# Kernel optimization log

Measured on AMD Instinct MI355X. Metric: run time of the kernel, lower is better.

## Reference

```python
import jax, jax.numpy as jnp
import numpy as np
import math

B, S, D, H = 2, 2048, 1024, 16
DK = D // H


def setup_inputs() -> dict:
    key = jax.random.key(0)
    ks = jax.random.split(key, 5)
    scale = 0.02
    x = jax.random.normal(ks[0], (B, S, D), dtype=jnp.float32)
    wq = jax.random.normal(ks[1], (D, D), dtype=jnp.float32) * scale
    wk = jax.random.normal(ks[2], (D, D), dtype=jnp.float32) * scale
    wv = jax.random.normal(ks[3], (D, D), dtype=jnp.float32) * scale
    wo = jax.random.normal(ks[4], (D, D), dtype=jnp.float32) * scale
    bq = jnp.zeros((D,), jnp.float32)
    bk = jnp.zeros((D,), jnp.float32)
    bv = jnp.zeros((D,), jnp.float32)
    bo = jnp.zeros((D,), jnp.float32)
    # causal mask: mask==0 positions are filled with -inf in the original
    mask = jnp.tril(jnp.ones((S, S), dtype=bool))[None, None]  # [1,1,S,S]
    return {"x": x, "mask": mask, "wq": wq, "bq": bq, "wk": wk, "bk": bk,
            "wv": wv, "bv": bv, "wo": wo, "bo": bo}


def reference(x, mask, wq, bq, wk, bk, wv, bv, wo, bo):
    b, sl, d = x.shape
    # torch Linear: y = x @ W^T + b
    def proj(w, bias):
        y = jnp.einsum('bsd,ed->bse', x, w) + bias
        return y.reshape(b, sl, H, DK).transpose(0, 2, 1, 3)  # [B,H,S,DK]
    q = proj(wq, bq)
    k = proj(wk, bk)
    v = proj(wv, bv)
    sc = jnp.einsum('bhqd,bhkd->bhqk', q, k) / math.sqrt(DK)  # [B,H,S,S]
    sc = jnp.where(mask, sc, -jnp.inf)
    aw = jax.nn.softmax(sc, axis=-1)
    # dropout is identity in eval mode (reference baseline)
    ao = jnp.einsum('bhqk,bhkd->bhqd', aw, v)
    ao = ao.transpose(0, 2, 1, 3).reshape(b, sl, d)
    out = jnp.einsum('bsd,ed->bse', ao, wo) + bo
    return out
```

## Files before the change

### kernel.cpp

```cpp
#include <hip/hip_runtime.h>
#include <cstdint>
#include <cstddef>

#define Bb 2
#define Ss 2048
#define Dd 1024
#define Hh 16
#define DKk 64

typedef unsigned short ushort_t;
typedef __bf16 bf16x8 __attribute__((ext_vector_type(8)));
typedef float f32x4 __attribute__((ext_vector_type(4)));
typedef unsigned short us8 __attribute__((ext_vector_type(8)));
typedef unsigned short us4 __attribute__((ext_vector_type(4)));

__device__ __forceinline__ ushort_t f2bf(float f) {
  __bf16 h = (__bf16)f;
  return __builtin_bit_cast(unsigned short, h);
}

__device__ __forceinline__ void gload_lds16(const void* g, void* l) {
  __builtin_amdgcn_global_load_lds(
      (__attribute__((address_space(1))) void*)(g),
      (__attribute__((address_space(3))) void*)(l),
      16, 0, 0);
}

__global__ __launch_bounds__(256) void cast_k(const float* __restrict__ s,
                                              ushort_t* __restrict__ d, int n8) {
  const int i = blockIdx.x * 256 + threadIdx.x;
  if (i >= n8) return;
  const float4* sp = (const float4*)s;
  float4 a = sp[2 * i], b = sp[2 * i + 1];
  us8 o;
  o[0] = f2bf(a.x); o[1] = f2bf(a.y); o[2] = f2bf(a.z); o[3] = f2bf(a.w);
  o[4] = f2bf(b.x); o[5] = f2bf(b.y); o[6] = f2bf(b.z); o[7] = f2bf(b.w);
  ((us8*)d)[i] = o;
}

template <int MODE>
__global__ __launch_bounds__(256) void gemm_k(
    const ushort_t* __restrict__ A, const ushort_t* __restrict__ W,
    const float* __restrict__ b0, const float* __restrict__ b1,
    const float* __restrict__ b2,
    ushort_t* __restrict__ oQ, ushort_t* __restrict__ oK,
    ushort_t* __restrict__ oVT, float* __restrict__ oF) {
  constexpr int Kd = 1024;
  __shared__ ushort_t As[128 * 32];
  __shared__ ushort_t Bs[128 * 32];
  const int tid = threadIdx.x;
  const int lane = tid & 63;
  const int wave = tid >> 6;
  const int m0 = blockIdx.y * 128;
  const int n0 = blockIdx.x * 128;
  const int lr = lane & 15;
  const int lg = lane >> 4;
  const int srow = lane >> 2;
  const int scol = (lane & 3) * 8;
  const int ar = (wave >> 1) * 64;
  const int bc = (wave & 1) * 64;

  f32x4 acc[4][4] = {};

  for (int kt = 0; kt < Kd / 32; ++kt) {
    const int k0 = kt * 32;
#pragma unroll
    for (int c = 0; c < 2; ++c) {
      const int seg = wave * 2 + c;
      const int row = seg * 16 + srow;
      gload_lds16(A + (size_t)(m0 + row) * Kd + k0 + scol, (char*)As + seg * 1024);
      gload_lds16(W + (size_t)(n0 + row) * Kd + k0 + scol, (char*)Bs + seg * 1024);
    }
    __syncthreads();
    bf16x8 af[4], bfr[4];
#pragma unroll
    for (int i = 0; i < 4; ++i)
      af[i] = *(const bf16x8*)&As[(ar + i * 16 + lr) * 32 + lg * 8];
#pragma unroll
    for (int j = 0; j < 4; ++j)
      bfr[j] = *(const bf16x8*)&Bs[(bc + j * 16 + lr) * 32 + lg * 8];
#pragma unroll
    for (int i = 0; i < 4; ++i)
#pragma unroll
      for (int j = 0; j < 4; ++j)
        acc[i][j] = __builtin_amdgcn_mfma_f32_16x16x32_bf16(af[i], bfr[j],
                                                            acc[i][j], 0, 0, 0);
    __syncthreads();
  }

#pragma unroll
  for (int i = 0; i < 4; ++i) {
    const int mrow = m0 + ar + i * 16 + lg * 4;
#pragma unroll
    for (int j = 0; j < 4; ++j) {
      const int n = n0 + bc + j * 16 + lr;
      if (MODE == 0) {
        const int sel = n >> 10;
        const int nn = n & 1023;
        const float bias = (sel == 0 ? b0 : sel == 1 ? b1 : b2)[nn];
        const int h = nn >> 6, dk = nn & 63;
        const int bidx = mrow >> 11;
        const int s = mrow & 2047;
        const int bh = bidx * Hh + h;
        if (sel == 2) {
          us4 pk;
#pragma unroll
          for (int r = 0; r < 4; ++r) pk[r] = f2bf(acc[i][j][r] + bias);
          *(us4*)&oVT[((size_t)bh * DKk + dk) * Ss + s] = pk;
        } else {
          ushort_t* dst = (sel == 0) ? oQ : oK;
          const float mul = (sel == 0) ? 0.1803368842f : 1.0f;
#pragma unroll
          for (int r = 0; r < 4; ++r)
            dst[((size_t)bh * Ss + (s + r)) * DKk + dk] =
                f2bf((acc[i][j][r] + bias) * mul);
        }
      } else {
        const float bias = b0[n];
#pragma unroll
        for (int r = 0; r < 4; ++r)
          oF[(size_t)(mrow + r) * Dd + n] = acc[i][j][r] + bias;
      }
    }
  }
}

__global__ __launch_bounds__(256, 4) void attn_k(const ushort_t* __restrict__ Qg,
                                                 const ushort_t* __restrict__ Kg,
                                                 const ushort_t* __restrict__ Vt,
                                                 ushort_t* __restrict__ AO) {
  __shared__ ushort_t Ks[2][64 * 64];
  __shared__ ushort_t Pl[4][16 * 72];
  const int tid = threadIdx.x, lane = tid & 63, wave = tid >> 6;
  const int bx = blockIdx.x;
  const int bh = bx & 31;
  const int r_ = bx >> 8;
  const int sub = (bx >> 5) & 7;
  const int g = (3 - r_) * 8 + ((r_ & 1) ? 7 - sub : sub);
  const int lr = lane & 15, lg = lane >> 4;
  const ushort_t* Qp = Qg + (size_t)bh * Ss * DKk;
  const ushort_t* Kp = Kg + (size_t)bh * Ss * DKk;
  const ushort_t* Vp = Vt + (size_t)bh * DKk * Ss;
  ushort_t* P = Pl[wave];
  const int s_row = lane >> 3;
  const int s_slot = (lane & 7) ^ s_row;
  const int sw = lr & 7;
  const int q0 = g * 64 + wave * 16;
  const int nt = g + 1;

  auto stageK = [&](int t, int buf) {
    const int rb = wave * 16;
#pragma unroll
    for (int c = 0; c < 2; ++c)
      gload_lds16(Kp + (size_t)(t * 64 + rb + c * 8 + s_row) * DKk + s_slot * 8,
                  &Ks[buf][(rb + c * 8) * 64]);
  };

  stageK(0, 0);

  bf16x8 qf[2];
#pragma unroll
  for (int ks = 0; ks < 2; ++ks)
    qf[ks] = *(const bf16x8*)&Qp[(size_t)(q0 + lr) * DKk + ks * 32 + lg * 8];

  f32x4 o[4] = {};
  float m_ = -3e38f, l_ = 0.f;

  __syncthreads();

  for (int t = 0; t < nt; ++t) {
    const int cb = t & 1;
    if (t + 1 < nt) stageK(t + 1, cb ^ 1);
    const int j0 = t * 64;
    const bool diag = (t == nt - 1);
    const int nct = diag ? wave + 1 : 4;

    bf16x8 vt[4][2];
#pragma unroll
    for (int dj = 0; dj < 4; ++dj)
#pragma unroll
      for (int ksp = 0; ksp < 2; ++ksp)
        vt[dj][ksp] = *(const bf16x8*)&Vp[(size_t)(dj * 16 + lr) * Ss + j0 +
                                          ksp * 32 + lg * 8];

    f32x4 sc[4];
#pragma unroll
    for (int ct = 0; ct < 4; ++ct) {
      if (ct < nct) {
        const int krow = ct * 16 + lr;
        const bf16x8 k0v = *(const bf16x8*)&Ks[cb][krow * 64 + ((lg ^ sw) * 8)];
        const bf16x8 k1v =
            *(const bf16x8*)&Ks[cb][krow * 64 + (((4 | lg) ^ sw) * 8)];
        f32x4 z = {};
        z = __builtin_amdgcn_mfma_f32_16x16x32_bf16(k0v, qf[0], z, 0, 0, 0);
        z = __builtin_amdgcn_mfma_f32_16x16x32_bf16(k1v, qf[1], z, 0, 0, 0);
        sc[ct] = z;
      }
    }
    if (diag) {
#pragma unroll
      for (int ct = 0; ct < 4; ++ct)
        if (ct == nct - 1)
#pragma unroll
          for (int r = 0; r < 4; ++r)
            if (lg * 4 + r > lr) sc[ct][r] = -1e30f;
    }

    float mx = -3e38f;
#pragma unroll
    for (int ct = 0; ct < 4; ++ct)
      if (ct < nct)
#pragma unroll
        for (int r = 0; r < 4; ++r) mx = fmaxf(mx, sc[ct][r]);
    mx = fmaxf(mx, __shfl_xor(mx, 16, 64));
    mx = fmaxf(mx, __shfl_xor(mx, 32, 64));
    const float mnew = fmaxf(m_, mx);
    const float fs = __builtin_exp2f(m_ - mnew);
    m_ = mnew;
    float ls = 0.f;
#pragma unroll
    for (int ct = 0; ct < 4; ++ct) {
      if (ct < nct) {
        float p0 = __builtin_exp2f(sc[ct][0] - mnew);
        float p1 = __builtin_exp2f(sc[ct][1] - mnew);
        float p2 = __builtin_exp2f(sc[ct][2] - mnew);
        float p3 = __builtin_exp2f(sc[ct][3] - mnew);
        ls += (p0 + p1) + (p2 + p3);
        us4 pk;
        pk[0] = f2bf(p0); pk[1] = f2bf(p1); pk[2] = f2bf(p2); pk[3] = f2bf(p3);
        *(us4*)&P[lr * 72 + ct * 16 + lg * 4] = pk;
      } else {
        us4 zz = {};
        *(us4*)&P[lr * 72 + ct * 16 + lg * 4] = zz;
      }
    }
    ls += __shfl_xor(ls, 16, 64);
    ls += __shfl_xor(ls, 32, 64);
    l_ = l_ * fs + ls;

    float fso[4];
#pragma unroll
    for (int r = 0; r < 4; ++r) fso[r] = __shfl(fs, lg * 4 + r, 64);
#pragma unroll
    for (int dj = 0; dj < 4; ++dj)
#pragma unroll
      for (int r = 0; r < 4; ++r) o[dj][r] *= fso[r];

    asm volatile("s_waitcnt lgkmcnt(0)" ::: "memory");
    bf16x8 pa[2];
#pragma unroll
    for (int ksp = 0; ksp < 2; ++ksp)
      pa[ksp] = *(const bf16x8*)&P[lr * 72 + ksp * 32 + lg * 8];
#pragma unroll
    for (int dj = 0; dj < 4; ++dj)
#pragma unroll
      for (int ksp = 0; ksp < 2; ++ksp)
        o[dj] = __builtin_amdgcn_mfma_f32_16x16x32_bf16(pa[ksp], vt[dj][ksp],
                                                        o[dj], 0, 0, 0);

    __syncthreads();
  }

  const int bb = bh >> 4, hh = bh & 15;
#pragma unroll
  for (int r = 0; r < 4; ++r) {
    const float lq = __shfl(l_, lg * 4 + r, 64);
    const float inv = 1.0f / lq;
    const size_t m = (size_t)bb * Ss + q0 + lg * 4 + r;
#pragma unroll
    for (int dj = 0; dj < 4; ++dj)
      AO[m * Dd + hh * 64 + dj * 16 + lr] = f2bf(o[dj][r] * inv);
  }
}

extern "C" void kernel_launch(void* const* d_in, const int* in_sizes, int n_in,
                              void* d_out, int out_size, void* d_ws, size_t ws_size,
                              hipStream_t stream) {
  const float* x  = (const float*)d_in[0];
  const float* wq = (const float*)d_in[2];
  const float* bq = (const float*)d_in[3];
  const float* wk = (const float*)d_in[4];
  const float* bk = (const float*)d_in[5];
  const float* wv = (const float*)d_in[6];
  const float* bv = (const float*)d_in[7];
  const float* wo = (const float*)d_in[8];
  const float* bo = (const float*)d_in[9];

  ushort_t* ws   = (ushort_t*)d_ws;
  ushort_t* xb   = ws;
  ushort_t* wqkv = xb + 4096 * 1024;
  ushort_t* wob  = wqkv + 3072 * 1024;
  ushort_t* Qb   = wob + 1024 * 1024;
  ushort_t* Kb   = Qb + 4194304;
  ushort_t* VTb  = Kb + 4194304;
  ushort_t* AOb  = xb;

  cast_k<<<2048, 256, 0, stream>>>(x, xb, 524288);
  cast_k<<<512, 256, 0, stream>>>(wq, wqkv, 131072);
  cast_k<<<512, 256, 0, stream>>>(wk, wqkv + 1048576, 131072);
  cast_k<<<512, 256, 0, stream>>>(wv, wqkv + 2097152, 131072);
  cast_k<<<512, 256, 0, stream>>>(wo, wob, 131072);

  gemm_k<0><<<dim3(24, 32), 256, 0, stream>>>(xb, wqkv, bq, bk, bv, Qb, Kb, VTb,
                                              nullptr);
  attn_k<<<1024, 256, 0, stream>>>(Qb, Kb, VTb, AOb);
  gemm_k<1><<<dim3(8, 32), 256, 0, stream>>>(AOb, wob, bo, nullptr, nullptr,
                                             nullptr, nullptr, nullptr,
                                             (float*)d_out);
}
```

Before: 151.2 us.

## Compute softmax row sums via MFMA and transpose PV output layout

Replaces the per-lane row-sum accumulation and cross-lane shuffles with an MFMA against a ones vector, which accumulates the softmax denominator directly in the accumulator layout. The PV MFMA operands are swapped so each lane holds a full query row in its accumulator. This removes the shuffles for rescale factors and denominators and allows a vectorized 4-element store of the output. It adds two extra MFMAs per tile and depends on the transposed accumulator layout matching the per-lane running max.

```diff
diff --git a/kernel.cpp b/kernel.cpp
--- a/kernel.cpp
+++ b/kernel.cpp
@@ -163,8 +163,13 @@
   for (int ks = 0; ks < 2; ++ks)
     qf[ks] = *(const bf16x8*)&Qp[(size_t)(q0 + lr) * DKk + ks * 32 + lg * 8];
 
+  bf16x8 onesv;
+#pragma unroll
+  for (int e = 0; e < 8; ++e) onesv[e] = (__bf16)1.0f;
+
   f32x4 o[4] = {};
-  float m_ = -3e38f, l_ = 0.f;
+  f32x4 l4 = {};
+  float m_ = -3e38f;
 
   __syncthreads();
 
@@ -217,15 +222,13 @@
     const float mnew = fmaxf(m_, mx);
     const float fs = __builtin_exp2f(m_ - mnew);
     m_ = mnew;
-    float ls = 0.f;
 #pragma unroll
     for (int ct = 0; ct < 4; ++ct) {
       if (ct < nct) {
-        float p0 = __builtin_exp2f(sc[ct][0] - mnew);
-        float p1 = __builtin_exp2f(sc[ct][1] - mnew);
-        float p2 = __builtin_exp2f(sc[ct][2] - mnew);
-        float p3 = __builtin_exp2f(sc[ct][3] - mnew);
-        ls += (p0 + p1) + (p2 + p3);
+        float p0 = __builtin_exp2f(sc[ct][0] - m_);
+        float p1 = __builtin_exp2f(sc[ct][1] - m_);
+        float p2 = __builtin_exp2f(sc[ct][2] - m_);
+        float p3 = __builtin_exp2f(sc[ct][3] - m_);
         us4 pk;
         pk[0] = f2bf(p0); pk[1] = f2bf(p1); pk[2] = f2bf(p2); pk[3] = f2bf(p3);
         *(us4*)&P[lr * 72 + ct * 16 + lg * 4] = pk;
@@ -234,42 +237,41 @@
         *(us4*)&P[lr * 72 + ct * 16 + lg * 4] = zz;
       }
     }
-    ls += __shfl_xor(ls, 16, 64);
-    ls += __shfl_xor(ls, 32, 64);
-    l_ = l_ * fs + ls;
-
-    float fso[4];
-#pragma unroll
-    for (int r = 0; r < 4; ++r) fso[r] = __shfl(fs, lg * 4 + r, 64);
+
 #pragma unroll
     for (int dj = 0; dj < 4; ++dj)
 #pragma unroll
-      for (int r = 0; r < 4; ++r) o[dj][r] *= fso[r];
+      for (int r = 0; r < 4; ++r) o[dj][r] *= fs;
+    l4[0] *= fs;
 
     asm volatile("s_waitcnt lgkmcnt(0)" ::: "memory");
     bf16x8 pa[2];
 #pragma unroll
     for (int ksp = 0; ksp < 2; ++ksp)
       pa[ksp] = *(const bf16x8*)&P[lr * 72 + ksp * 32 + lg * 8];
+
+#pragma unroll
+    for (int ksp = 0; ksp < 2; ++ksp)
+      l4 = __builtin_amdgcn_mfma_f32_16x16x32_bf16(onesv, pa[ksp], l4, 0, 0, 0);
 #pragma unroll
     for (int dj = 0; dj < 4; ++dj)
 #pragma unroll
       for (int ksp = 0; ksp < 2; ++ksp)
-        o[dj] = __builtin_amdgcn_mfma_f32_16x16x32_bf16(pa[ksp], vt[dj][ksp],
+        o[dj] = __builtin_amdgcn_mfma_f32_16x16x32_bf16(vt[dj][ksp], pa[ksp],
                                                         o[dj], 0, 0, 0);
 
     __syncthreads();
   }
 
   const int bb = bh >> 4, hh = bh & 15;
-#pragma unroll
-  for (int r = 0; r < 4; ++r) {
-    const float lq = __shfl(l_, lg * 4 + r, 64);
-    const float inv = 1.0f / lq;
-    const size_t m = (size_t)bb * Ss + q0 + lg * 4 + r;
-#pragma unroll
-    for (int dj = 0; dj < 4; ++dj)
-      AO[m * Dd + hh * 64 + dj * 16 + lr] = f2bf(o[dj][r] * inv);
+  const float inv = 1.0f / l4[0];
+#pragma unroll
+  for (int dj = 0; dj < 4; ++dj) {
+    us4 pk;
+#pragma unroll
+    for (int r = 0; r < 4; ++r) pk[r] = f2bf(o[dj][r] * inv);
+    *(us4*)&AO[((size_t)bb * Ss + q0 + lr) * Dd + hh * 64 + dj * 16 + lg * 4] =
+        pk;
   }
 }
 
```

Result: no change. 151.7 us (+0.4%).
